# Kernel optimization log

Measured on AMD Instinct MI355X. Metric: run time of the kernel, lower is better.

Reference implementation:

```python
import jax, jax.numpy as jnp
import numpy as np
import math

L, B, S, D, H, FF = 6, 4, 1024, 1024, 16, 4096
HD = D // H
EPS = 1e-5


def _ln(x, g, b):
    m = jnp.mean(x, axis=-1, keepdims=True)
    v = jnp.mean(jnp.square(x - m), axis=-1, keepdims=True)
    return (x - m) / jnp.sqrt(v + EPS) * g + b


def setup_inputs() -> dict:
    key = jax.random.key(0)
    ks = jax.random.split(key, 8)
    std = 0.02
    inp = {
        'x': jax.random.normal(ks[0], (B, S, D), jnp.float32),
        'lengths': jax.random.randint(ks[1], (B,), S // 2, S + 1),
        'rel_bias': jax.random.normal(ks[2], (H, S, S), jnp.float32) * std,
        'ln1_g': jnp.ones((L, D), jnp.float32),
        'ln1_b': jnp.zeros((L, D), jnp.float32),
        'qkv_w': jax.random.normal(ks[3], (L, D, 3 * D), jnp.float32) * std,
        'qkv_b': jnp.zeros((L, 3 * D), jnp.float32),
        'out_w': jax.random.normal(ks[4], (L, D, D), jnp.float32) * std,
        'out_b': jnp.zeros((L, D), jnp.float32),
        'ln2_g': jnp.ones((L, D), jnp.float32),
        'ln2_b': jnp.zeros((L, D), jnp.float32),
        'fc1_w': jax.random.normal(ks[5], (L, D, FF), jnp.float32) * std,
        'fc1_b': jnp.zeros((L, FF), jnp.float32),
        'fc2_w': jax.random.normal(ks[6], (L, FF, D), jnp.float32) * std,
        'fc2_b': jnp.zeros((L, D), jnp.float32),
    }
    return inp


def reference(x, lengths, rel_bias, ln1_g, ln1_b, qkv_w, qkv_b, out_w, out_b,
              ln2_g, ln2_b, fc1_w, fc1_b, fc2_w, fc2_b):
    # causal additive mask [S,S]: -inf above the diagonal (torch.triu diagonal=1)
    ar = jnp.arange(S)
    causal = jnp.where(ar[None, :] > ar[:, None], -jnp.inf, 0.0).astype(x.dtype)
    # key padding mask [B,S]: True where position is padding
    pad = ar[None, :] >= lengths[:, None]
    scale = 1.0 / math.sqrt(HD)

    for i in range(L):
        # --- attention sub-block (pre-LN) ---
        xn = _ln(x, ln1_g[i], ln1_b[i])
        qkv = xn @ qkv_w[i] + qkv_b[i]                      # [B,S,3D]
        q, k, v = jnp.split(qkv, 3, axis=-1)
        q = q.reshape(B, S, H, HD)
        k = k.reshape(B, S, H, HD)
        v = v.reshape(B, S, H, HD)
        scores = jnp.einsum('bqhd,bkhd->bhqk', q, k) * scale  # [B,H,S,S]
        scores = scores + rel_bias[None] + causal[None, None]
        scores = jnp.where(pad[:, None, None, :], -jnp.inf, scores)
        attn = jax.nn.softmax(scores, axis=-1)
        o = jnp.einsum('bhqk,bkhd->bqhd', attn, v).reshape(B, S, D)
        o = o @ out_w[i] + out_b[i]
        o = jnp.where(pad[:, :, None], 0.0, o)
        x = x + o
        # --- feed-forward sub-block (LN inside FF, residual outside) ---
        h = _ln(x, ln2_g[i], ln2_b[i])
        h = jax.nn.gelu(h @ fc1_w[i] + fc1_b[i], approximate=False)
        h = h @ fc2_w[i] + fc2_b[i]
        x = x + h
    return x
```

## Files before the change

### kernel.cpp

```cpp
#include <hip/hip_runtime.h>
#include <cstdint>
#include <cstddef>

constexpr int L_ = 6, B_ = 4, S_ = 1024, D_ = 1024, H_ = 16, FF_ = 4096;
constexpr int D3_ = 3 * D_;
constexpr int HD_ = D_ / H_;

typedef float f32x4 __attribute__((ext_vector_type(4)));
typedef __bf16 bf16x8 __attribute__((ext_vector_type(8)));
typedef unsigned short u16;
typedef u16 u16x4 __attribute__((ext_vector_type(4)));
typedef u16 u16x8 __attribute__((ext_vector_type(8)));

__device__ __forceinline__ u16 f2bf(float f) {
    union { float f; uint32_t u; } v; v.f = f;
    uint32_t r = v.u + 0x7FFFu + ((v.u >> 16) & 1u);
    return (u16)(r >> 16);
}

__global__ __launch_bounds__(256) void cvt_transpose(
    const float* __restrict__ W, u16* __restrict__ WT, int K, int N)
{
    __shared__ float tile[64][65];
    const int tid = threadIdx.x;
    const int bn = blockIdx.x * 64, bk = blockIdx.y * 64;
    #pragma unroll
    for (int i = 0; i < 16; ++i) {
        int idx = i * 256 + tid;
        int r = idx >> 6, c = idx & 63;
        tile[r][c] = W[(size_t)(bk + r) * N + bn + c];
    }
    __syncthreads();
    #pragma unroll
    for (int i = 0; i < 16; ++i) {
        int idx = i * 256 + tid;
        int r = idx >> 6, c = idx & 63;
        WT[(size_t)(bn + r) * K + bk + c] = f2bf(tile[c][r]);
    }
}

__global__ __launch_bounds__(256) void vt_transpose(
    const u16* __restrict__ qkv, u16* __restrict__ vt)
{
    __shared__ u16 tile[64][72];
    const int tid = threadIdx.x;
    const int s0 = blockIdx.x * 64, bh = blockIdx.y;
    const int b = bh >> 4, h = bh & 15;
    #pragma unroll
    for (int i = 0; i < 2; ++i) {
        int idx = tid + i * 256;
        int r = idx >> 3, c8 = (idx & 7) * 8;
        u16x8 v = *(const u16x8*)(qkv + ((size_t)(b * S_ + s0 + r)) * D3_ + 2 * D_ + h * 64 + c8);
        #pragma unroll
        for (int j = 0; j < 8; ++j) tile[c8 + j][r] = v[j];
    }
    __syncthreads();
    #pragma unroll
    for (int i = 0; i < 2; ++i) {
        int idx = tid + i * 256;
        int r = idx >> 3, c8 = (idx & 7) * 8;
        u16x8 v;
        #pragma unroll
        for (int j = 0; j < 8; ++j) v[j] = tile[r][c8 + j];
        *(u16x8*)(vt + ((size_t)(bh * 64 + r)) * S_ + s0 + c8) = v;
    }
}

__global__ __launch_bounds__(256) void ln_kernel(
    const float* __restrict__ X, const float* __restrict__ g,
    const float* __restrict__ bp, u16* __restrict__ out)
{
    const int row = blockIdx.x, tid = threadIdx.x;
    const float* xr = X + (size_t)row * D_;
    f32x4 v = *(const f32x4*)(xr + tid * 4);
    float s  = v[0] + v[1] + v[2] + v[3];
    float s2 = v[0]*v[0] + v[1]*v[1] + v[2]*v[2] + v[3]*v[3];
    #pragma unroll
    for (int off = 32; off >= 1; off >>= 1) {
        s  += __shfl_down(s,  off);
        s2 += __shfl_down(s2, off);
    }
    __shared__ float red[8];
    const int lane = tid & 63, wid = tid >> 6;
    if (lane == 0) { red[wid] = s; red[4 + wid] = s2; }
    __syncthreads();
    s  = red[0] + red[1] + red[2] + red[3];
    s2 = red[4] + red[5] + red[6] + red[7];
    float mean = s * (1.f / D_);
    float var  = s2 * (1.f / D_) - mean * mean;
    float rstd = rsqrtf(var + 1e-5f);
    f32x4 gv = *(const f32x4*)(g  + tid * 4);
    f32x4 bv = *(const f32x4*)(bp + tid * 4);
    u16x4 o4;
    #pragma unroll
    for (int r = 0; r < 4; ++r) o4[r] = f2bf((v[r] - mean) * rstd * gv[r] + bv[r]);
    *(u16x4*)(out + (size_t)row * D_ + tid * 4) = o4;
}

template<int MODE>
__global__ __launch_bounds__(256) void gemm_bt(
    const u16* __restrict__ A, const u16* __restrict__ BT,
    const float* __restrict__ bias,
    u16* __restrict__ Cb, float* __restrict__ X,
    const int* __restrict__ lengths,
    int M, int N, int K)
{
    __shared__ __align__(16) u16 lA[128 * 32];
    __shared__ __align__(16) u16 lB[128 * 32];
    const int tid = threadIdx.x;
    const int lane = tid & 63;
    const int grp = lane >> 4, l15 = lane & 15;
    const int wid = tid >> 6;
    const int wm = wid >> 1, wn = wid & 1;
    const int m0 = blockIdx.y * 128, n0 = blockIdx.x * 128;

    const int srow = tid >> 2, sgg = tid & 3;
    const size_t aoff = (size_t)(m0 + srow) * K + sgg * 8;
    const size_t boff = (size_t)(n0 + srow) * K + sgg * 8;
    char* lAw = (char*)lA + srow * 64 + ((sgg * 16) ^ ((srow & 3) << 4));
    char* lBw = (char*)lB + srow * 64 + ((sgg * 16) ^ ((srow & 3) << 4));

    f32x4 acc[4][4] = {};
    bf16x8 ra0 = *(const bf16x8*)(A  + aoff);
    bf16x8 ra1 = *(const bf16x8*)(A  + aoff + (size_t)64 * K);
    bf16x8 rb0 = *(const bf16x8*)(BT + boff);
    bf16x8 rb1 = *(const bf16x8*)(BT + boff + (size_t)64 * K);

    for (int kk = 0; kk < K; kk += 32) {
        __syncthreads();
        *(bf16x8*)lAw          = ra0;
        *(bf16x8*)(lAw + 4096) = ra1;
        *(bf16x8*)lBw          = rb0;
        *(bf16x8*)(lBw + 4096) = rb1;
        __syncthreads();
        if (kk + 32 < K) {
            ra0 = *(const bf16x8*)(A  + aoff + kk + 32);
            ra1 = *(const bf16x8*)(A  + aoff + (size_t)64 * K + kk + 32);
            rb0 = *(const bf16x8*)(BT + boff + kk + 32);
            rb1 = *(const bf16x8*)(BT + boff + (size_t)64 * K + kk + 32);
        }
        bf16x8 af[4], bfr[4];
        #pragma unroll
        for (int mf = 0; mf < 4; ++mf) {
            int r = wm * 64 + mf * 16 + l15;
            af[mf] = *(const bf16x8*)((const char*)lA + r * 64 + ((grp * 16) ^ ((r & 3) << 4)));
        }
        #pragma unroll
        for (int nf = 0; nf < 4; ++nf) {
            int r = wn * 64 + nf * 16 + l15;
            bfr[nf] = *(const bf16x8*)((const char*)lB + r * 64 + ((grp * 16) ^ ((r & 3) << 4)));
        }
        #pragma unroll
        for (int mf = 0; mf < 4; ++mf)
            #pragma unroll
            for (int nf = 0; nf < 4; ++nf)
                acc[mf][nf] = __builtin_amdgcn_mfma_f32_16x16x32_bf16(af[mf], bfr[nf], acc[mf][nf], 0, 0, 0);
    }

    #pragma unroll
    for (int mf = 0; mf < 4; ++mf) {
        int row_g = m0 + wm * 64 + mf * 16 + grp * 4;
        #pragma unroll
        for (int nf = 0; nf < 4; ++nf) {
            int col_g = n0 + wn * 64 + nf * 16 + l15;
            float bv = bias[col_g];
            f32x4 v = acc[mf][nf];
            if constexpr (MODE == 0) {
                #pragma unroll
                for (int r = 0; r < 4; ++r)
                    Cb[(size_t)(row_g + r) * N + col_g] = f2bf(v[r] + bv);
            } else if constexpr (MODE == 2) {
                #pragma unroll
                for (int r = 0; r < 4; ++r) {
                    float t = v[r] + bv;
                    float ge = 0.5f * t * (1.f + erff(t * 0.70710678118654752f));
                    Cb[(size_t)(row_g + r) * N + col_g] = f2bf(ge);
                }
            } else if constexpr (MODE == 1) {
                #pragma unroll
                for (int r = 0; r < 4; ++r) {
                    int row = row_g + r;
                    int bidx = row >> 10, sp = row & 1023;
                    float add = (sp >= lengths[bidx]) ? 0.f : (v[r] + bv);
                    X[(size_t)row * N + col_g] += add;
                }
            } else {
                #pragma unroll
                for (int r = 0; r < 4; ++r)
                    X[(size_t)(row_g + r) * N + col_g] += v[r] + bv;
            }
        }
    }
}

__global__ __launch_bounds__(256) void attn_kernel(
    const u16* __restrict__ qkv,
    const u16* __restrict__ vt,
    const float* __restrict__ rel_bias,
    const int* __restrict__ lengths,
    u16* __restrict__ obuf)
{
    __shared__ __align__(16) char kls[64 * 128];
    __shared__ __align__(16) char vls[64 * 128];
    const int tid = threadIdx.x, lane = tid & 63, wid = tid >> 6;
    const int grp = lane >> 4, l15 = lane & 15;
    const int qt = blockIdx.x, bh = blockIdx.y;
    const int b = bh >> 4, h = bh & 15;
    const int len = lengths[b];
    const int qrow = qt * 64 + wid * 16 + l15;

    bf16x8 qf[2];
    {
        const u16* qp = qkv + ((size_t)(b * S_ + qrow)) * D3_ + h * 64 + grp * 8;
        qf[0] = *(const bf16x8*)qp;
        qf[1] = *(const bf16x8*)(qp + 32);
    }
    f32x4 oacc[4] = {};
    float m_run = -INFINITY, lsum = 0.f;
    int kt_end = (len + 63) >> 6;
    if (qt + 1 < kt_end) kt_end = qt + 1;

    for (int kt = 0; kt < kt_end; ++kt) {
        __syncthreads();
        #pragma unroll
        for (int i = 0; i < 2; ++i) {
            int id2 = tid + i * 256;
            int r = id2 >> 3, gg = id2 & 7;
            int sw = (r & 7) << 4;
            bf16x8 kv = *(const bf16x8*)(qkv + ((size_t)(b * S_ + kt * 64 + r)) * D3_ + D_ + h * 64 + gg * 8);
            *(bf16x8*)(kls + r * 128 + ((gg * 16) ^ sw)) = kv;
            bf16x8 vv = *(const bf16x8*)(vt + ((size_t)(bh * 64 + r)) * S_ + kt * 64 + gg * 8);
            *(bf16x8*)(vls + r * 128 + ((gg * 16) ^ sw)) = vv;
        }
        __syncthreads();

        f32x4 sf[4] = {};
        #pragma unroll
        for (int f = 0; f < 4; ++f) {
            int r = f * 16 + l15;
            int sw = (r & 7) << 4;
            #pragma unroll
            for (int t = 0; t < 2; ++t) {
                bf16x8 af = *(const bf16x8*)(kls + r * 128 + (((t * 32 + grp * 8) * 2) ^ sw));
                sf[f] = __builtin_amdgcn_mfma_f32_16x16x32_bf16(af, qf[t], sf[f], 0, 0, 0);
            }
        }
        float p[4][4];
        float tmax = -INFINITY;
        #pragma unroll
        for (int f = 0; f < 4; ++f) {
            f32x4 bi = *(const f32x4*)(rel_bias + ((size_t)h * S_ + qrow) * S_ + kt * 64 + f * 16 + grp * 4);
            #pragma unroll
            for (int r = 0; r < 4; ++r) {
                int kp = kt * 64 + f * 16 + grp * 4 + r;
                bool valid = (kp <= qrow) && (kp < len);
                float sv = valid ? fmaf(sf[f][r], 0.125f, bi[r]) : -INFINITY;
                p[f][r] = sv;
                tmax = fmaxf(tmax, sv);
            }
        }
        tmax = fmaxf(tmax, __shfl_xor(tmax, 16));
        tmax = fmaxf(tmax, __shfl_xor(tmax, 32));
        float m_new = fmaxf(m_run, tmax);
        float alpha = expf(m_run - m_new);
        float psum = 0.f;
        #pragma unroll
        for (int f = 0; f < 4; ++f)
            #pragma unroll
            for (int r = 0; r < 4; ++r) {
                float e = expf(p[f][r] - m_new);
                p[f][r] = e; psum += e;
            }
        psum += __shfl_xor(psum, 16);
        psum += __shfl_xor(psum, 32);
        lsum = lsum * alpha + psum;
        m_run = m_new;
        #pragma unroll
        for (int fo = 0; fo < 4; ++fo) {
            oacc[fo][0] *= alpha; oacc[fo][1] *= alpha;
            oacc[fo][2] *= alpha; oacc[fo][3] *= alpha;
        }
        #pragma unroll
        for (int t = 0; t < 2; ++t) {
            union { u16 u[8]; bf16x8 v; } pb;
            #pragma unroll
            for (int j = 0; j < 4; ++j) {
                pb.u[j]     = f2bf(p[2 * t][j]);
                pb.u[4 + j] = f2bf(p[2 * t + 1][j]);
            }
            #pragma unroll
            for (int fo = 0; fo < 4; ++fo) {
                int r = fo * 16 + l15;
                int sw = (r & 7) << 4;
                union { u16x4 h4[2]; bf16x8 v; } av;
                av.h4[0] = *(const u16x4*)(vls + r * 128 + ((t * 64 + grp * 8)      ^ sw));
                av.h4[1] = *(const u16x4*)(vls + r * 128 + ((t * 64 + grp * 8 + 32) ^ sw));
                oacc[fo] = __builtin_amdgcn_mfma_f32_16x16x32_bf16(av.v, pb.v, oacc[fo], 0, 0, 0);
            }
        }
    }
    float inv = 1.f / lsum;
    #pragma unroll
    for (int fo = 0; fo < 4; ++fo)
        #pragma unroll
        for (int r = 0; r < 4; ++r) {
            int hd = fo * 16 + grp * 4 + r;
            obuf[((size_t)(b * S_) + qrow) * D_ + h * 64 + hd] = f2bf(oacc[fo][r] * inv);
        }
}

extern "C" void kernel_launch(void* const* d_in, const int* in_sizes, int n_in,
                              void* d_out, int out_size, void* d_ws, size_t ws_size,
                              hipStream_t stream)
{
    const float* x_in     = (const float*)d_in[0];
    const int*   lengths  = (const int*)d_in[1];
    const float* rel_bias = (const float*)d_in[2];
    const float* ln1_g    = (const float*)d_in[3];
    const float* ln1_b    = (const float*)d_in[4];
    const float* qkv_w    = (const float*)d_in[5];
    const float* qkv_b    = (const float*)d_in[6];
    const float* out_w    = (const float*)d_in[7];
    const float* out_b    = (const float*)d_in[8];
    const float* ln2_g    = (const float*)d_in[9];
    const float* ln2_b    = (const float*)d_in[10];
    const float* fc1_w    = (const float*)d_in[11];
    const float* fc1_b    = (const float*)d_in[12];
    const float* fc2_w    = (const float*)d_in[13];
    const float* fc2_b    = (const float*)d_in[14];
    float* X = (float*)d_out;

    char* ws = (char*)d_ws;
    size_t off = 0;
    auto alloc = [&](size_t bytes) {
        char* p = ws + off;
        off = (off + bytes + 255) & ~(size_t)255;
        return p;
    };
    u16* wT_qkv = (u16*)alloc((size_t)D3_ * D_ * 2);
    u16* wT_out = (u16*)alloc((size_t)D_ * D_ * 2);
    u16* wT_fc1 = (u16*)alloc((size_t)FF_ * D_ * 2);
    u16* wT_fc2 = (u16*)alloc((size_t)D_ * FF_ * 2);
    u16* xn     = (u16*)alloc((size_t)B_ * S_ * D_ * 2);
    u16* qkvb   = (u16*)alloc((size_t)B_ * S_ * D3_ * 2);
    u16* vtb    = (u16*)alloc((size_t)B_ * H_ * HD_ * S_ * 2);
    u16* ob     = (u16*)alloc((size_t)B_ * S_ * D_ * 2);
    u16* h1     = (u16*)alloc((size_t)B_ * S_ * FF_ * 2);

    const int M = B_ * S_;

    hipMemcpyAsync(X, x_in, (size_t)M * D_ * sizeof(float),
                   hipMemcpyDeviceToDevice, stream);

    for (int i = 0; i < L_; ++i) {
        cvt_transpose<<<dim3(D3_ / 64, D_ / 64), 256, 0, stream>>>(
            qkv_w + (size_t)i * D_ * D3_, wT_qkv, D_, D3_);
        cvt_transpose<<<dim3(D_ / 64, D_ / 64), 256, 0, stream>>>(
            out_w + (size_t)i * D_ * D_, wT_out, D_, D_);
        cvt_transpose<<<dim3(FF_ / 64, D_ / 64), 256, 0, stream>>>(
            fc1_w + (size_t)i * D_ * FF_, wT_fc1, D_, FF_);
        cvt_transpose<<<dim3(D_ / 64, FF_ / 64), 256, 0, stream>>>(
            fc2_w + (size_t)i * FF_ * D_, wT_fc2, FF_, D_);

        ln_kernel<<<M, 256, 0, stream>>>(X, ln1_g + i * D_, ln1_b + i * D_, xn);
        gemm_bt<0><<<dim3(D3_ / 128, M / 128), 256, 0, stream>>>(
            xn, wT_qkv, qkv_b + (size_t)i * D3_, qkvb, nullptr, nullptr, M, D3_, D_);
        vt_transpose<<<dim3(S_ / 64, B_ * H_), 256, 0, stream>>>(qkvb, vtb);
        attn_kernel<<<dim3(S_ / 64, B_ * H_), 256, 0, stream>>>(
            qkvb, vtb, rel_bias, lengths, ob);
        gemm_bt<1><<<dim3(D_ / 128, M / 128), 256, 0, stream>>>(
            ob, wT_out, out_b + (size_t)i * D_, nullptr, X, lengths, M, D_, D_);

        ln_kernel<<<M, 256, 0, stream>>>(X, ln2_g + i * D_, ln2_b + i * D_, xn);
        gemm_bt<2><<<dim3(FF_ / 128, M / 128), 256, 0, stream>>>(
            xn, wT_fc1, fc1_b + (size_t)i * FF_, h1, nullptr, nullptr, M, FF_, D_);
        gemm_bt<3><<<dim3(D_ / 128, M / 128), 256, 0, stream>>>(
            h1, wT_fc2, fc2_b + (size_t)i * D_, nullptr, X, nullptr, M, D_, FF_);
    }
}
```

Measured before the change: 1.838 ms.

## Use direct global-to-LDS loads and split-K with atomic adds for narrow GEMMs

The GEMM now stages A and B tiles with global_load_lds builtins straight into shared memory, using a new XOR swizzle, instead of going through registers. The register prefetch double-buffering is dropped. The out-projection and fc2 GEMMs split K in two along gridDim.z and accumulate into the residual with float atomicAdd, applying bias only in the first split. This raises block count for the 256-block narrow GEMMs, at the cost of atomic traffic, nondeterministic summation order and less load/compute overlap.

```diff
diff --git a/kernel.cpp b/kernel.cpp
--- a/kernel.cpp
+++ b/kernel.cpp
@@ -16,6 +16,13 @@
     union { float f; uint32_t u; } v; v.f = f;
     uint32_t r = v.u + 0x7FFFu + ((v.u >> 16) & 1u);
     return (u16)(r >> 16);
+}
+
+__device__ __forceinline__ void gload16(const void* g, void* l) {
+    __builtin_amdgcn_global_load_lds(
+        (const __attribute__((address_space(1))) unsigned int*)g,
+        (__attribute__((address_space(3))) unsigned int*)l,
+        16, 0, 0);
 }
 
 __global__ __launch_bounds__(256) void cvt_transpose(
@@ -113,57 +120,53 @@
     const int wid = tid >> 6;
     const int wm = wid >> 1, wn = wid & 1;
     const int m0 = blockIdx.y * 128, n0 = blockIdx.x * 128;
-
-    const int srow = tid >> 2, sgg = tid & 3;
-    const size_t aoff = (size_t)(m0 + srow) * K + sgg * 8;
-    const size_t boff = (size_t)(n0 + srow) * K + sgg * 8;
-    char* lAw = (char*)lA + srow * 64 + ((sgg * 16) ^ ((srow & 3) << 4));
-    char* lBw = (char*)lB + srow * 64 + ((sgg * 16) ^ ((srow & 3) << 4));
+    const int Kh = K / gridDim.z;
+    const int k0 = blockIdx.z * Kh;
+
+    const int lrow = lane >> 2;
+    const int cchunk = (lane & 3) ^ ((lane >> 3) & 3);
+    const u16* gA = A  + (size_t)(m0 + wid * 32 + lrow) * K + k0 + cchunk * 8;
+    const u16* gB = BT + (size_t)(n0 + wid * 32 + lrow) * K + k0 + cchunk * 8;
+    char* lAw = (char*)lA + wid * 2048;
+    char* lBw = (char*)lB + wid * 2048;
+    const size_t rstep = (size_t)16 * K;
+
+    const int rslot = (grp ^ ((l15 >> 1) & 3)) * 16;
 
     f32x4 acc[4][4] = {};
-    bf16x8 ra0 = *(const bf16x8*)(A  + aoff);
-    bf16x8 ra1 = *(const bf16x8*)(A  + aoff + (size_t)64 * K);
-    bf16x8 rb0 = *(const bf16x8*)(BT + boff);
-    bf16x8 rb1 = *(const bf16x8*)(BT + boff + (size_t)64 * K);
-
-    for (int kk = 0; kk < K; kk += 32) {
+    for (int kk = 0; kk < Kh; kk += 32) {
+        gload16(gA + kk,         lAw);
+        gload16(gA + kk + rstep, lAw + 1024);
+        gload16(gB + kk,         lBw);
+        gload16(gB + kk + rstep, lBw + 1024);
         __syncthreads();
-        *(bf16x8*)lAw          = ra0;
-        *(bf16x8*)(lAw + 4096) = ra1;
-        *(bf16x8*)lBw          = rb0;
-        *(bf16x8*)(lBw + 4096) = rb1;
-        __syncthreads();
-        if (kk + 32 < K) {
-            ra0 = *(const bf16x8*)(A  + aoff + kk + 32);
-            ra1 = *(const bf16x8*)(A  + aoff + (size_t)64 * K + kk + 32);
-            rb0 = *(const bf16x8*)(BT + boff + kk + 32);
-            rb1 = *(const bf16x8*)(BT + boff + (size_t)64 * K + kk + 32);
-        }
         bf16x8 af[4], bfr[4];
         #pragma unroll
         for (int mf = 0; mf < 4; ++mf) {
             int r = wm * 64 + mf * 16 + l15;
-            af[mf] = *(const bf16x8*)((const char*)lA + r * 64 + ((grp * 16) ^ ((r & 3) << 4)));
+            af[mf] = *(const bf16x8*)((const char*)lA + r * 64 + rslot);
         }
         #pragma unroll
         for (int nf = 0; nf < 4; ++nf) {
             int r = wn * 64 + nf * 16 + l15;
-            bfr[nf] = *(const bf16x8*)((const char*)lB + r * 64 + ((grp * 16) ^ ((r & 3) << 4)));
+            bfr[nf] = *(const bf16x8*)((const char*)lB + r * 64 + rslot);
         }
         #pragma unroll
         for (int mf = 0; mf < 4; ++mf)
             #pragma unroll
             for (int nf = 0; nf < 4; ++nf)
                 acc[mf][nf] = __builtin_amdgcn_mfma_f32_16x16x32_bf16(af[mf], bfr[nf], acc[mf][nf], 0, 0, 0);
-    }
-
+        __syncthreads();
+    }
+
+    const float bscale = (k0 == 0) ? 1.f : 0.f;
     #pragma unroll
     for (int mf = 0; mf < 4; ++mf) {
         int row_g = m0 + wm * 64 + mf * 16 + grp * 4;
         #pragma unroll
         for (int nf = 0; nf < 4; ++nf) {
             int col_g = n0 + wn * 64 + nf * 16 + l15;
-            float bv = bias[col_g];
+            float bv = bias[col_g] * bscale;
             f32x4 v = acc[mf][nf];
             if constexpr (MODE == 0) {
                 #pragma unroll
@@ -177,17 +180,17 @@
                     Cb[(size_t)(row_g + r) * N + col_g] = f2bf(ge);
                 }
             } else if constexpr (MODE == 1) {
+                int len = lengths[row_g >> 10];
                 #pragma unroll
                 for (int r = 0; r < 4; ++r) {
                     int row = row_g + r;
-                    int bidx = row >> 10, sp = row & 1023;
-                    float add = (sp >= lengths[bidx]) ? 0.f : (v[r] + bv);
-                    X[(size_t)row * N + col_g] += add;
+                    float add = ((row & 1023) >= len) ? 0.f : (v[r] + bv);
+                    atomicAdd(&X[(size_t)row * N + col_g], add);
                 }
             } else {
                 #pragma unroll
                 for (int r = 0; r < 4; ++r)
-                    X[(size_t)(row_g + r) * N + col_g] += v[r] + bv;
+                    atomicAdd(&X[(size_t)(row_g + r) * N + col_g], v[r] + bv);
             }
         }
     }
@@ -363,18 +366,18 @@
             fc2_w + (size_t)i * FF_ * D_, wT_fc2, FF_, D_);
 
         ln_kernel<<<M, 256, 0, stream>>>(X, ln1_g + i * D_, ln1_b + i * D_, xn);
-        gemm_bt<0><<<dim3(D3_ / 128, M / 128), 256, 0, stream>>>(
+        gemm_bt<0><<<dim3(D3_ / 128, M / 128, 1), 256, 0, stream>>>(
             xn, wT_qkv, qkv_b + (size_t)i * D3_, qkvb, nullptr, nullptr, M, D3_, D_);
         vt_transpose<<<dim3(S_ / 64, B_ * H_), 256, 0, stream>>>(qkvb, vtb);
         attn_kernel<<<dim3(S_ / 64, B_ * H_), 256, 0, stream>>>(
             qkvb, vtb, rel_bias, lengths, ob);
-        gemm_bt<1><<<dim3(D_ / 128, M / 128), 256, 0, stream>>>(
+        gemm_bt<1><<<dim3(D_ / 128, M / 128, 2), 256, 0, stream>>>(
             ob, wT_out, out_b + (size_t)i * D_, nullptr, X, lengths, M, D_, D_);
 
         ln_kernel<<<M, 256, 0, stream>>>(X, ln2_g + i * D_, ln2_b + i * D_, xn);
-        gemm_bt<2><<<dim3(FF_ / 128, M / 128), 256, 0, stream>>>(
+        gemm_bt<2><<<dim3(FF_ / 128, M / 128, 1), 256, 0, stream>>>(
             xn, wT_fc1, fc1_b + (size_t)i * FF_, h1, nullptr, nullptr, M, FF_, D_);
-        gemm_bt<3><<<dim3(D_ / 128, M / 128), 256, 0, stream>>>(
+        gemm_bt<3><<<dim3(D_ / 128, M / 128, 2), 256, 0, stream>>>(
             h1, wT_fc2, fc2_b + (size_t)i * D_, nullptr, X, nullptr, M, D_, FF_);
     }
 }
```

New measurement: 1.944 ms. +5.8%, slower.
